# Kernel optimization log

Measured on AMD Instinct MI355X. Metric: run time of the kernel, lower is better.

Reference implementation:

```python
import jax, jax.numpy as jnp
import numpy as np

BS = 64
NUM_SHARED = 32
IN_DIM = 32
OUT_DIM = 64
H = 16
W_SP = 16
NUM_OUT = 64
ROUTE_NUM = 3
NUM_IN = NUM_SHARED * H * W_SP  # 8192


def squash(s):
    # s: [bs, num_out_caps, out_dim]; norm over dim=2 (matches torch vec.norm(dim=2))
    norm = jnp.linalg.norm(s, axis=2, keepdims=True)
    norm_sq = norm * norm
    coeff = norm_sq / (1.0 + norm_sq) / norm
    return s * coeff


def setup_inputs() -> dict:
    key = jax.random.key(0)
    k1, k2 = jax.random.split(key)
    x = jax.random.normal(k1, (BS, NUM_SHARED * IN_DIM, H, W_SP), dtype=jnp.float32)
    # nn.Linear(in_dim, out_dim, bias=False) weight: [out_dim, in_dim], one per shared group
    W = jax.random.normal(k2, (NUM_SHARED, OUT_DIM, IN_DIM), dtype=jnp.float32) * 0.05
    return {"x": x, "W": W}


def reference(x, W):
    bs = x.shape[0]
    # torch: input.view(bs, num_shared, -1, in_dim) -- row-major reinterpretation
    u = x.reshape(bs, NUM_SHARED, H * W_SP, IN_DIM)
    # per-group linear: y = u @ W_s^T  -> pred: [bs, num_in_caps, out_dim]
    pred = jnp.einsum('bspi,soi->bspo', u, W).reshape(bs, NUM_IN, OUT_DIM)
    # b_init == 'zero'
    b = jnp.zeros((bs, NUM_OUT, NUM_IN), dtype=x.dtype)
    v = None
    for _ in range(ROUTE_NUM):
        c = jax.nn.softmax(b, axis=1)                       # softmax over out-caps axis
        s = jnp.einsum('bon,bnd->bod', c, pred)             # [bs, O, out_dim]
        v = squash(s)
        # v0 path: delta_b is NOT detached
        delta_b = jnp.einsum('bnd,bod->bon', pred, v)       # [bs, O, N]
        b = b + delta_b
    return v
```

## Files before the change

### kernel.cpp

```cpp
#include <hip/hip_runtime.h>
#include <math.h>


#define NSH     32
#define IN_DIM_ 32
#define OUT_DIM_ 64
#define BS_     64

__global__ __launch_bounds__(256) void k_reduce(const float* __restrict__ x,
                                                float* __restrict__ U) {
    const int blk = blockIdx.x;
    const float* xb = x + (size_t)blk * 8192;
    const int t  = threadIdx.x;
    const int i4 = t & 7;
    const int pl = t >> 3;

    float4 a = make_float4(0.f, 0.f, 0.f, 0.f);
#pragma unroll
    for (int k = 0; k < 8; ++k) {
        const float4 v = *reinterpret_cast<const float4*>(
            xb + (size_t)(pl + 32 * k) * IN_DIM_ + i4 * 4);
        a.x += v.x; a.y += v.y; a.z += v.z; a.w += v.w;
    }

    __shared__ float4 red[256];
    red[t] = a;
    __syncthreads();
#pragma unroll
    for (int st = 128; st >= 8; st >>= 1) {
        if (t < st) {
            const float4 o = red[t + st];
            red[t].x += o.x; red[t].y += o.y; red[t].z += o.z; red[t].w += o.w;
        }
        __syncthreads();
    }
    if (t < 8) {
        *reinterpret_cast<float4*>(U + (size_t)blk * IN_DIM_ + t * 4) = red[t];
    }
}

__global__ __launch_bounds__(256) void k_finish(const float* __restrict__ U,
                                                const float* __restrict__ W,
                                                float* __restrict__ out) {
    const int b = blockIdx.x;
    const int t = threadIdx.x;

    __shared__ float Ub[NSH * IN_DIM_];
#pragma unroll
    for (int q = 0; q < 4; ++q) Ub[t + 256 * q] = U[(size_t)b * 1024 + t + 256 * q];
    __syncthreads();

    const int d  = t & 63;
    const int sg = t >> 6;

    float acc = 0.f;
#pragma unroll
    for (int ss = 0; ss < 8; ++ss) {
        const int s = sg * 8 + ss;
        const float4* W4 = reinterpret_cast<const float4*>(
            W + (size_t)s * OUT_DIM_ * IN_DIM_ + (size_t)d * IN_DIM_);
        const float4* U4 = reinterpret_cast<const float4*>(Ub + s * IN_DIM_);
#pragma unroll
        for (int q = 0; q < 8; ++q) {
            const float4 w = W4[q];
            const float4 u = U4[q];
            acc += w.x * u.x + w.y * u.y + w.z * u.z + w.w * u.w;
        }
    }

    __shared__ float red[256];
    red[t] = acc;
    __syncthreads();

    __shared__ float vsh[OUT_DIM_];
    if (t < 64) {
        const float s1 = (red[t] + red[t + 64] + red[t + 128] + red[t + 192])
                         * (1.0f / 64.0f);
        float sq = s1 * s1;
#pragma unroll
        for (int off = 32; off >= 1; off >>= 1) sq += __shfl_xor(sq, off, 64);
        const float norm  = sqrtf(sq);
        const float coeff = norm / (1.0f + sq);
        vsh[t] = s1 * coeff;
    }
    __syncthreads();

    float* ob = out + (size_t)b * (OUT_DIM_ * OUT_DIM_);
    const float val = vsh[t & 63];
#pragma unroll
    for (int q = 0; q < 16; ++q) ob[t + 256 * q] = val;
}

extern "C" void kernel_launch(void* const* d_in, const int* in_sizes, int n_in,
                              void* d_out, int out_size, void* d_ws, size_t ws_size,
                              hipStream_t stream) {
    const float* x = (const float*)d_in[0];
    const float* W = (const float*)d_in[1];
    float* out = (float*)d_out;
    float* U   = (float*)d_ws;

    k_reduce<<<BS_ * NSH, 256, 0, stream>>>(x, U);
    k_finish<<<BS_, 256, 0, stream>>>(U, W, out);
}
```

Before: 99.80 us.

## Fuse capsule reduction and projection into one 1024-thread kernel per batch

```diff
diff --git a/kernel.cpp b/kernel.cpp
--- a/kernel.cpp
+++ b/kernel.cpp
@@ -2,93 +2,106 @@
 #include <math.h>
 
 
-#define NSH     32
-#define IN_DIM_ 32
-#define OUT_DIM_ 64
-#define BS_     64
+__global__ __launch_bounds__(1024) void k_caplayer(const float* __restrict__ x,
+                                                   const float* __restrict__ W,
+                                                   float* __restrict__ out) {
+    const int b  = blockIdx.x;
+    const int t  = threadIdx.x;
+    const int w  = t >> 6;
+    const int ln = t & 63;
 
-__global__ __launch_bounds__(256) void k_reduce(const float* __restrict__ x,
-                                                float* __restrict__ U) {
-    const int blk = blockIdx.x;
-    const float* xb = x + (size_t)blk * 8192;
-    const int t  = threadIdx.x;
-    const int i4 = t & 7;
-    const int pl = t >> 3;
+    __shared__ float U[32][32];
+    __shared__ float pb[2048];
+    __shared__ float vsh[64];
 
-    float4 a = make_float4(0.f, 0.f, 0.f, 0.f);
+    const float4* base = reinterpret_cast<const float4*>(x) + (size_t)b * 65536;
+    const float4* c0 = base + (size_t)(2 * w) * 2048 + ln;
+    const float4* c1 = c0 + 2048;
+    float4 a0 = make_float4(0.f, 0.f, 0.f, 0.f);
+    float4 a1 = make_float4(0.f, 0.f, 0.f, 0.f);
 #pragma unroll
-    for (int k = 0; k < 8; ++k) {
-        const float4 v = *reinterpret_cast<const float4*>(
-            xb + (size_t)(pl + 32 * k) * IN_DIM_ + i4 * 4);
-        a.x += v.x; a.y += v.y; a.z += v.z; a.w += v.w;
+    for (int kb = 0; kb < 4; ++kb) {
+        float4 t0[8], t1[8];
+#pragma unroll
+        for (int j = 0; j < 8; ++j) t0[j] = c0[(size_t)64 * (8 * kb + j)];
+#pragma unroll
+        for (int j = 0; j < 8; ++j) t1[j] = c1[(size_t)64 * (8 * kb + j)];
+#define SUM8C(T, c) ((((T[0].c + T[1].c) + (T[2].c + T[3].c)) + \
+                      ((T[4].c + T[5].c) + (T[6].c + T[7].c))))
+        a0.x += SUM8C(t0, x); a0.y += SUM8C(t0, y);
+        a0.z += SUM8C(t0, z); a0.w += SUM8C(t0, w);
+        a1.x += SUM8C(t1, x); a1.y += SUM8C(t1, y);
+        a1.z += SUM8C(t1, z); a1.w += SUM8C(t1, w);
+#undef SUM8C
     }
-
-    __shared__ float4 red[256];
-    red[t] = a;
-    __syncthreads();
 #pragma unroll
-    for (int st = 128; st >= 8; st >>= 1) {
-        if (t < st) {
-            const float4 o = red[t + st];
-            red[t].x += o.x; red[t].y += o.y; red[t].z += o.z; red[t].w += o.w;
-        }
-        __syncthreads();
+    for (int off = 8; off <= 32; off <<= 1) {
+        a0.x += __shfl_xor(a0.x, off, 64);
+        a0.y += __shfl_xor(a0.y, off, 64);
+        a0.z += __shfl_xor(a0.z, off, 64);
+        a0.w += __shfl_xor(a0.w, off, 64);
+        a1.x += __shfl_xor(a1.x, off, 64);
+        a1.y += __shfl_xor(a1.y, off, 64);
+        a1.z += __shfl_xor(a1.z, off, 64);
+        a1.w += __shfl_xor(a1.w, off, 64);
     }
-    if (t < 8) {
-        *reinterpret_cast<float4*>(U + (size_t)blk * IN_DIM_ + t * 4) = red[t];
+    if (ln < 8) {
+        *reinterpret_cast<float4*>(&U[2 * w][4 * ln])     = a0;
+        *reinterpret_cast<float4*>(&U[2 * w + 1][4 * ln]) = a1;
     }
-}
-
-__global__ __launch_bounds__(256) void k_finish(const float* __restrict__ U,
-                                                const float* __restrict__ W,
-                                                float* __restrict__ out) {
-    const int b = blockIdx.x;
-    const int t = threadIdx.x;
-
-    __shared__ float Ub[NSH * IN_DIM_];
-#pragma unroll
-    for (int q = 0; q < 4; ++q) Ub[t + 256 * q] = U[(size_t)b * 1024 + t + 256 * q];
     __syncthreads();
 
-    const int d  = t & 63;
-    const int sg = t >> 6;
-
-    float acc = 0.f;
+    const int i4 = ln & 7;
+    const float4 u0 = *reinterpret_cast<const float4*>(&U[2 * w][4 * i4]);
+    const float4 u1 = *reinterpret_cast<const float4*>(&U[2 * w + 1][4 * i4]);
+    const float4* Ws = reinterpret_cast<const float4*>(W) + (size_t)(2 * w) * 512 + ln;
+    float p[16];
 #pragma unroll
-    for (int ss = 0; ss < 8; ++ss) {
-        const int s = sg * 8 + ss;
-        const float4* W4 = reinterpret_cast<const float4*>(
-            W + (size_t)s * OUT_DIM_ * IN_DIM_ + (size_t)d * IN_DIM_);
-        const float4* U4 = reinterpret_cast<const float4*>(Ub + s * IN_DIM_);
+    for (int j = 0; j < 8; ++j) {
+        const float4 w4 = Ws[64 * j];
+        p[j] = w4.x * u0.x + w4.y * u0.y + w4.z * u0.z + w4.w * u0.w;
+    }
 #pragma unroll
-        for (int q = 0; q < 8; ++q) {
-            const float4 w = W4[q];
-            const float4 u = U4[q];
-            acc += w.x * u.x + w.y * u.y + w.z * u.z + w.w * u.w;
-        }
+    for (int j = 0; j < 8; ++j) {
+        const float4 w4 = Ws[512 + 64 * j];
+        p[8 + j] = w4.x * u1.x + w4.y * u1.y + w4.z * u1.z + w4.w * u1.w;
     }
-
-    __shared__ float red[256];
-    red[t] = acc;
+#pragma unroll
+    for (int j = 0; j < 16; ++j) {
+        p[j] += __shfl_xor(p[j], 1, 64);
+        p[j] += __shfl_xor(p[j], 2, 64);
+        p[j] += __shfl_xor(p[j], 4, 64);
+    }
+    if (i4 == 0) {
+        const int dbase = ln >> 3;
+#pragma unroll
+        for (int j = 0; j < 8; ++j) pb[(2 * w) * 64 + dbase + 8 * j] = p[j];
+#pragma unroll
+        for (int j = 0; j < 8; ++j) pb[(2 * w + 1) * 64 + dbase + 8 * j] = p[8 + j];
+    }
     __syncthreads();
 
-    __shared__ float vsh[OUT_DIM_];
+    pb[t] += pb[t + 1024];
+    __syncthreads();
+    if (t < 512) pb[t] += pb[t + 512];
+    __syncthreads();
+    if (t < 256) pb[t] += pb[t + 256];
+    __syncthreads();
+    if (t < 128) pb[t] += pb[t + 128];
+    __syncthreads();
     if (t < 64) {
-        const float s1 = (red[t] + red[t + 64] + red[t + 128] + red[t + 192])
-                         * (1.0f / 64.0f);
+        const float tot = pb[t] + pb[t + 64];
+        const float s1  = tot * (1.0f / 64.0f);
         float sq = s1 * s1;
 #pragma unroll
         for (int off = 32; off >= 1; off >>= 1) sq += __shfl_xor(sq, off, 64);
-        const float norm  = sqrtf(sq);
-        const float coeff = norm / (1.0f + sq);
+        const float coeff = sqrtf(sq) / (1.0f + sq);
         vsh[t] = s1 * coeff;
     }
     __syncthreads();
 
-    float* ob = out + (size_t)b * (OUT_DIM_ * OUT_DIM_);
-    const float val = vsh[t & 63];
-#pragma unroll
-    for (int q = 0; q < 16; ++q) ob[t + 256 * q] = val;
+    float4* ob4 = reinterpret_cast<float4*>(out + (size_t)b * 4096);
+    ob4[t] = *reinterpret_cast<const float4*>(&vsh[(4 * t) & 63]);
 }
 
 extern "C" void kernel_launch(void* const* d_in, const int* in_sizes, int n_in,
@@ -97,8 +110,7 @@
     const float* x = (const float*)d_in[0];
     const float* W = (const float*)d_in[1];
     float* out = (float*)d_out;
-    float* U   = (float*)d_ws;
+    (void)d_ws; (void)ws_size;
 
-    k_reduce<<<BS_ * NSH, 256, 0, stream>>>(x, U);
-    k_finish<<<BS_, 256, 0, stream>>>(U, W, out);
+    k_caplayer<<<64, 1024, 0, stream>>>(x, W, out);
 }
```

After: 106.8 us. 1.07x slower.
